# Kernel optimization log

Measured on AMD Instinct MI355X. Metric: run time of the kernel, lower is better.

The kernel has to match this reference:

```python
import jax, jax.numpy as jnp
import numpy as np

B, N_OBJ, N_VAL, E, H, HEADS = 512, 10, 200, 420, 128, 4
NPG = 1 + N_OBJ + N_VAL  # nodes per graph = 211
N = B * NPG
FMIN = float(np.finfo(np.float32).min)


def _gat_conv(x, src, dst, W, att_src, att_dst, bias, concat):
    # PyG GATConv (v1): linear (no bias) -> per-head attention logits ->
    # leaky_relu(a_src[j]+a_dst[i]) -> softmax over edges grouped by dst -> scatter-sum
    heads = att_src.shape[0]
    xs = (x @ W).reshape(N, heads, -1)            # [N, heads, C]
    a_src = (xs * att_src).sum(-1)                # [N, heads]
    a_dst = (xs * att_dst).sum(-1)                # [N, heads]
    alpha = jax.nn.leaky_relu(a_src[src] + a_dst[dst], 0.2)   # [Etot, heads]
    amax = jax.ops.segment_max(alpha, dst, num_segments=N)
    ex = jnp.exp(alpha - amax[dst])
    denom = jax.ops.segment_sum(ex, dst, num_segments=N)
    alpha = ex / (denom[dst] + 1e-16)
    out = jax.ops.segment_sum(xs[src] * alpha[..., None], dst, num_segments=N)  # [N,heads,C]
    out = out.reshape(N, -1) if concat else out.mean(axis=1)
    return out + bias


def setup_inputs() -> dict:
    key = jax.random.key(0)
    ks = jax.random.split(key, 24)
    s = 0.1
    C1 = H // HEADS  # 32
    inp = {
        'head_node': jax.random.normal(ks[0], (B, 2), jnp.float32),
        'objective_nodes': jax.random.normal(ks[1], (B, N_OBJ, 2), jnp.float32),
        'value_nodes': jax.random.normal(ks[2], (B, N_VAL, 5), jnp.float32),
        'edge_indices': jax.random.randint(ks[3], (B, 2, E), 0, NPG, jnp.int64 if jax.config.jax_enable_x64 else jnp.int32),
        'accept_mask': jnp.ones((B, 2), jnp.float32),
        'W_head': jax.random.normal(ks[4], (2, H)) * s, 'b_head': jnp.zeros((H,)),
        'W_obj': jax.random.normal(ks[5], (2, H)) * s, 'b_obj': jnp.zeros((H,)),
        'W_val': jax.random.normal(ks[6], (5, H)) * s, 'b_val': jnp.zeros((H,)),
        'W1': jax.random.normal(ks[7], (H, HEADS * C1)) * s,
        'att_src1': jax.random.normal(ks[8], (HEADS, C1)) * s,
        'att_dst1': jax.random.normal(ks[9], (HEADS, C1)) * s,
        'b1': jnp.zeros((HEADS * C1,)),
        'W2': jax.random.normal(ks[10], (H, HEADS * H)) * s,
        'att_src2': jax.random.normal(ks[11], (HEADS, H)) * s,
        'att_dst2': jax.random.normal(ks[12], (HEADS, H)) * s,
        'b2': jnp.zeros((H,)),
        'W_acc': jax.random.normal(ks[13], (H, 2)) * 0.01, 'b_acc': jnp.zeros((2,)),
        'W_off': jax.random.normal(ks[14], (H, 1)) * 0.01, 'b_off': jnp.zeros((1,)),
        'W_vf': jax.random.normal(ks[15], (H, 1)) * s, 'b_vf': jnp.zeros((1,)),
    }
    return inp


def reference(head_node, objective_nodes, value_nodes, edge_indices, accept_mask,
              W_head, b_head, W_obj, b_obj, W_val, b_val,
              W1, att_src1, att_dst1, b1, W2, att_src2, att_dst2, b2,
              W_acc, b_acc, W_off, b_off, W_vf, b_vf):
    # node encoders + ReLU
    h_head = jax.nn.relu(head_node @ W_head + b_head)                  # [B,H]
    h_obj = jax.nn.relu(objective_nodes @ W_obj + b_obj)               # [B,N_OBJ,H]
    h_val = jax.nn.relu(value_nodes @ W_val + b_val)                   # [B,N_VAL,H]
    h_nodes = jnp.concatenate([h_head[:, None], h_obj, h_val], axis=1)  # [B,NPG,H]
    x = h_nodes.reshape(N, H)
    # batch graphs: offset per-graph edge indices, add self loops
    offs = (jnp.arange(B, dtype=edge_indices.dtype) * NPG)[:, None, None]
    ei = (edge_indices + offs).transpose(1, 0, 2).reshape(2, -1)       # [2, B*E]
    loops = jnp.arange(N, dtype=edge_indices.dtype)
    src = jnp.concatenate([ei[0], loops])
    dst = jnp.concatenate([ei[1], loops])
    # GAT: layer1 concat heads, ReLU (BasicGNN inter-layer act), layer2 mean heads
    x1 = jax.nn.relu(_gat_conv(x, src, dst, W1, att_src1, att_dst1, b1, True))
    x2 = _gat_conv(x1, src, dst, W2, att_src2, att_dst2, b2, False)
    h_out = jax.nn.relu(x2).reshape(B, NPG, H)
    h_head_out = h_out[:, 0]                                           # [B,H]
    h_val_out = h_out[:, -N_VAL:]                                      # [B,N_VAL,H]
    offer_logits = (h_val_out @ W_off + b_off).squeeze(-1)             # [B,N_VAL]
    accept_inf_mask = jnp.maximum(jnp.log(accept_mask), FMIN)
    accept_logits = h_head_out @ W_acc + b_acc + accept_inf_mask       # [B,2]
    vf = h_head_out @ W_vf + b_vf                                      # [B,1]
    return jnp.concatenate([accept_logits, offer_logits, vf], axis=-1)  # [B, 2+N_VAL+1]
```

## Files before the change

kernel.cpp:

```cpp
#include <hip/hip_runtime.h>

typedef unsigned short u16;
typedef unsigned int u32;
typedef short short8 __attribute__((ext_vector_type(8)));
typedef float f32x4 __attribute__((ext_vector_type(4)));

#define NB   512
#define NPG  211
#define NOBJ 10
#define NVAL 200
#define NE   420
#define NN   (NB * NPG)

__device__ __forceinline__ float bf2f(u16 u){
  union { unsigned i; float f; } v; v.i = ((unsigned)u) << 16; return v.f;
}
__device__ __forceinline__ u16 f2bf(float f){
  union { float f; unsigned i; } v; v.f = f;
  return (u16)((v.i + 0x7FFFu + ((v.i >> 16) & 1u)) >> 16);
}
__device__ __forceinline__ float lo_bf(u32 u){ union{u32 i;float f;}v; v.i=u<<16; return v.f; }
__device__ __forceinline__ float hi_bf(u32 u){ union{u32 i;float f;}v; v.i=u&0xffff0000u; return v.f; }
__device__ __forceinline__ u32 pack_bf(float a, float b){ return (u32)f2bf(a) | ((u32)f2bf(b)<<16); }
__device__ __forceinline__ float lrelu(float s){ return s > 0.f ? s : 0.2f * s; }
__device__ __forceinline__ short8 pack8(ushort4 a, ushort4 b){
  short8 v;
  v[0]=(short)a.x; v[1]=(short)a.y; v[2]=(short)a.z; v[3]=(short)a.w;
  v[4]=(short)b.x; v[5]=(short)b.y; v[6]=(short)b.z; v[7]=(short)b.w;
  return v;
}
__device__ __forceinline__ int swz(int r, int c){
  return (r << 7) + (((c & ~3) ^ ((r & 15) << 2)) | (c & 3));
}

__global__ __launch_bounds__(256) void k_prept(const float* __restrict__ W1, const float* __restrict__ W2,
                                               u16* __restrict__ W1t, u16* __restrict__ W2t){
  int gid = blockIdx.x * 256 + threadIdx.x;
  if (gid < 16384){
    int k = gid >> 7, n = gid & 127;
    W1t[n * 128 + k] = f2bf(W1[k * 128 + n]);
  } else {
    int t = gid - 16384;
    int n = t >> 9, kk = t & 511;
    int h = kk >> 7, c = kk & 127;
    W2t[n * 512 + kk] = f2bf(W2[c * 512 + h * 128 + n]);
  }
}

__global__ __launch_bounds__(256) void k_prepwm(const float* __restrict__ W2, const float* __restrict__ as2,
                                                const float* __restrict__ ad2,
                                                float* __restrict__ wms, float* __restrict__ wmd){
  int gid = blockIdx.x * 256 + threadIdx.x;
  int which = gid >> 9, hk = gid & 511;
  int h = hk >> 7, k = hk & 127;
  const float* av = which ? ad2 : as2;
  float s = 0.f;
  for (int j = 0; j < 128; ++j)
    s += W2[k * 512 + h * 128 + j] * av[h * 128 + j];
  (which ? wmd : wms)[hk] = s;
}

__global__ __launch_bounds__(1024, 1) void k_graph(
    const float* __restrict__ head, const float* __restrict__ obj, const float* __restrict__ val,
    const int* __restrict__ eidx, const float* __restrict__ amask,
    const float* __restrict__ Wh, const float* __restrict__ bh,
    const float* __restrict__ Wo, const float* __restrict__ bo,
    const float* __restrict__ Wv, const float* __restrict__ bv,
    const u16* __restrict__ W1t, const float* __restrict__ as1, const float* __restrict__ ad1,
    const float* __restrict__ b1,
    const u16* __restrict__ W2t, const float* __restrict__ wms, const float* __restrict__ wmd,
    const float* __restrict__ b2,
    const float* __restrict__ Wacc, const float* __restrict__ bacc,
    const float* __restrict__ Woff, const float* __restrict__ boff,
    const float* __restrict__ Wvf,  const float* __restrict__ bvf,
    float* __restrict__ out)
{
  __shared__ __align__(16) char sm[135008];
  u16*   sX   = (u16*)sm;
  u16*   sY   = (u16*)(sm + 54016);
  float* sLs  = (float*)(sm + 108032);
  float* sLd  = (float*)(sm + 111408);
  float* sW   = (float*)(sm + 114784);
  float* sDen = (float*)(sm + 124896);
  int*   sEs  = (int*)(sm + 128272);
  int*   sEd  = (int*)(sm + 129952);
  int*   sOff = (int*)(sm + 131632);
  int*   sSrc = (int*)(sm + 132480);

  const int b    = blockIdx.x;
  const int tid  = threadIdx.x;
  const int lane = tid & 63;
  const int wv   = tid >> 6;
  const int l15  = lane & 15;
  const int lg   = lane >> 4;
  const int cp   = lane << 1;
  const int cHi  = cp & ~3, cLo = cp & 3;
  const int hh   = lane >> 4;

  int tmi[4], tcb[4]; bool tact[4];
  #pragma unroll
  for (int s = 0; s < 4; ++s){
    int t = wv + (s << 4);
    tact[s] = t < 56; tmi[s] = t >> 2; tcb[s] = (t & 3) << 5;
  }

  const int* eg = eidx + (size_t)b * 2 * NE;
  if (tid < NE){ sEs[tid] = eg[tid]; sEd[tid] = eg[NE + tid]; }
  else if (tid >= 512 && tid < 640)      sDen[tid - 512] = as1[tid - 512];
  else if (tid >= 640 && tid < 768)      sDen[tid - 512] = ad1[tid - 640];

  for (int it = tid; it < NPG * 32; it += 1024){
    int n = it >> 5, cc = (it & 31) << 2;
    float a[4];
    if (n == 0){
      const float* in = head + (size_t)b * 2;
      float i0 = in[0], i1 = in[1];
      #pragma unroll
      for (int t = 0; t < 4; ++t){ int c = cc + t; a[t] = bh[c] + i0 * Wh[c] + i1 * Wh[128 + c]; }
    } else if (n <= NOBJ){
      const float* in = obj + ((size_t)b * NOBJ + (n - 1)) * 2;
      float i0 = in[0], i1 = in[1];
      #pragma unroll
      for (int t = 0; t < 4; ++t){ int c = cc + t; a[t] = bo[c] + i0 * Wo[c] + i1 * Wo[128 + c]; }
    } else {
      const float* in = val + ((size_t)b * NVAL + (n - 11)) * 5;
      float f[5];
      #pragma unroll
      for (int k = 0; k < 5; ++k) f[k] = in[k];
      #pragma unroll
      for (int t = 0; t < 4; ++t){
        int c = cc + t; float s = bv[c];
        #pragma unroll
        for (int k = 0; k < 5; ++k) s += f[k] * Wv[k * 128 + c];
        a[t] = s;
      }
    }
    ushort4 u;
    u.x = f2bf(fmaxf(a[0], 0.f)); u.y = f2bf(fmaxf(a[1], 0.f));
    u.z = f2bf(fmaxf(a[2], 0.f)); u.w = f2bf(fmaxf(a[3], 0.f));
    *(ushort4*)&sX[swz(n, cc)] = u;
  }
  __syncthreads();

  if (tid < NPG){
    int c = 1;
    const int4* p4 = (const int4*)sEd;
    #pragma unroll 4
    for (int i = 0; i < NE / 4; ++i){
      int4 v = p4[i];
      c += (v.x == tid) + (v.y == tid) + (v.z == tid) + (v.w == tid);
    }
    sOff[tid] = c;
  }
  __syncthreads();
  {
    int deg = (tid < NPG) ? sOff[tid] : 0;
    int v = deg;
    #pragma unroll
    for (int st = 1; st < 256; st <<= 1){
      if (tid < 256) sSrc[tid] = v;
      __syncthreads();
      if (tid < 256 && tid >= st) v += sSrc[tid - st];
      __syncthreads();
    }
    if (tid < NPG) sOff[tid] = v - deg;
    if (tid == NPG - 1) sOff[NPG] = v;
  }
  __syncthreads();
  if (tid < NPG){
    int p = sOff[tid];
    sSrc[p++] = tid;
    const int4* pd4 = (const int4*)sEd;
    const int4* ps4 = (const int4*)sEs;
    for (int i = 0; i < NE / 4; ++i){
      int4 d = pd4[i]; int4 s = ps4[i];
      if (d.x == tid) sSrc[p++] = s.x;
      if (d.y == tid) sSrc[p++] = s.y;
      if (d.z == tid) sSrc[p++] = s.z;
      if (d.w == tid) sSrc[p++] = s.w;
    }
  }
  __syncthreads();

  {
    f32x4 acc[4][2];
    #pragma unroll
    for (int s = 0; s < 4; ++s){ acc[s][0] = (f32x4){0,0,0,0}; acc[s][1] = (f32x4){0,0,0,0}; }
    #pragma unroll
    for (int kk = 0; kk < 4; ++kk){
      int k0 = kk * 32 + (lg << 2);
      #pragma unroll
      for (int s = 0; s < 4; ++s) if (tact[s]){
        const u16* B0 = W1t + (size_t)(tcb[s] + l15) * 128 + k0;
        const u16* B1 = W1t + (size_t)(tcb[s] + 16 + l15) * 128 + k0;
        short8 bf0 = pack8(*(const ushort4*)B0, *(const ushort4*)(B0 + 16));
        short8 bf1 = pack8(*(const ushort4*)B1, *(const ushort4*)(B1 + 16));
        int rr = tmi[s] * 16 + l15; rr = rr < NPG ? rr : NPG - 1;
        short8 af = pack8(*(const ushort4*)&sX[swz(rr, k0)],
                          *(const ushort4*)&sX[swz(rr, k0 + 16)]);
        acc[s][0] = __builtin_amdgcn_mfma_f32_16x16x32_bf16(af, bf0, acc[s][0], 0, 0, 0);
        acc[s][1] = __builtin_amdgcn_mfma_f32_16x16x32_bf16(af, bf1, acc[s][1], 0, 0, 0);
      }
    }
    #pragma unroll
    for (int s = 0; s < 4; ++s) if (tact[s]){
      int r0 = tmi[s] * 16 + (lg << 2);
      #pragma unroll
      for (int ct = 0; ct < 2; ++ct){
        int col = tcb[s] + ct * 16 + l15;
        #pragma unroll
        for (int r = 0; r < 4; ++r){
          int row = r0 + r;
          if (row < NPG) sY[swz(row, col)] = f2bf(acc[s][ct][r]);
        }
      }
    }
  }
  __syncthreads();

  if (tid < NPG * 4){
    int n = tid >> 2, h = tid & 3;
    float s = 0.f, d = 0.f;
    #pragma unroll
    for (int j = 0; j < 8; ++j){
      int c = h * 32 + j * 4;
      ushort4 xv = *(const ushort4*)&sY[swz(n, c)];
      #pragma unroll
      for (int t = 0; t < 4; ++t){
        float xf = bf2f(((const u16*)&xv)[t]);
        s += xf * sDen[c + t];
        d += xf * sDen[128 + c + t];
      }
    }
    sLs[tid] = s; sLd[tid] = d;
  }
  __syncthreads();

  if (tid < NPG * 4){
    int dst = tid >> 2, h = tid & 3;
    int o0 = sOff[dst], o1 = sOff[dst + 1];
    float ad = sLd[tid];
    float m = -3e38f;
    int e = o0;
    for (; e + 4 <= o1; e += 4){
      int s0 = sSrc[e], s1 = sSrc[e+1], s2 = sSrc[e+2], s3 = sSrc[e+3];
      float l0 = sLs[s0*4+h], l1 = sLs[s1*4+h], l2 = sLs[s2*4+h], l3 = sLs[s3*4+h];
      m = fmaxf(m, fmaxf(fmaxf(lrelu(l0+ad), lrelu(l1+ad)), fmaxf(lrelu(l2+ad), lrelu(l3+ad))));
    }
    for (; e < o1; ++e) m = fmaxf(m, lrelu(sLs[sSrc[e]*4+h] + ad));
    float dn = 0.f;
    e = o0;
    for (; e + 4 <= o1; e += 4){
      int s0 = sSrc[e], s1 = sSrc[e+1], s2 = sSrc[e+2], s3 = sSrc[e+3];
      float e0 = __expf(lrelu(sLs[s0*4+h]+ad) - m);
      float e1 = __expf(lrelu(sLs[s1*4+h]+ad) - m);
      float e2 = __expf(lrelu(sLs[s2*4+h]+ad) - m);
      float e3 = __expf(lrelu(sLs[s3*4+h]+ad) - m);
      sW[h*632+e] = e0; sW[h*632+e+1] = e1; sW[h*632+e+2] = e2; sW[h*632+e+3] = e3;
      dn += (e0 + e1) + (e2 + e3);
    }
    for (; e < o1; ++e){
      float ee = __expf(lrelu(sLs[sSrc[e]*4+h]+ad) - m);
      sW[h*632+e] = ee; dn += ee;
    }
    sDen[h * 211 + dst] = 1.0f / (dn + 1e-16f);
  }
  __syncthreads();

  {
    const float b1v0 = b1[cp], b1v1 = b1[cp + 1];
    const float* wp  = sW + hh * 632;
    const float* dnp = sDen + hh * 211;
    for (int dst = wv; dst < NPG; dst += 16){
      int o0 = sOff[dst], o1 = sOff[dst + 1];
      float a0 = 0.f, a1 = 0.f;
      int e = o0;
      for (; e + 4 <= o1; e += 4){
        int s0 = sSrc[e], s1 = sSrc[e+1], s2 = sSrc[e+2], s3 = sSrc[e+3];
        u32 f0 = *(const u32*)&sY[(s0<<7) + (cHi ^ ((s0&15)<<2)) + cLo];
        u32 f1 = *(const u32*)&sY[(s1<<7) + (cHi ^ ((s1&15)<<2)) + cLo];
        u32 f2 = *(const u32*)&sY[(s2<<7) + (cHi ^ ((s2&15)<<2)) + cLo];
        u32 f3 = *(const u32*)&sY[(s3<<7) + (cHi ^ ((s3&15)<<2)) + cLo];
        float w0 = wp[e], w1 = wp[e+1], w2 = wp[e+2], w3 = wp[e+3];
        a0 += w0*lo_bf(f0) + w1*lo_bf(f1) + w2*lo_bf(f2) + w3*lo_bf(f3);
        a1 += w0*hi_bf(f0) + w1*hi_bf(f1) + w2*hi_bf(f2) + w3*hi_bf(f3);
      }
      for (; e < o1; ++e){
        int sn = sSrc[e];
        u32 f = *(const u32*)&sY[(sn<<7) + (cHi ^ ((sn&15)<<2)) + cLo];
        float w = wp[e];
        a0 += w * lo_bf(f); a1 += w * hi_bf(f);
      }
      float r = dnp[dst];
      *(u32*)&sX[(dst<<7) + (cHi ^ ((dst&15)<<2)) + cLo] =
        pack_bf(fmaxf(a0 * r + b1v0, 0.f), fmaxf(a1 * r + b1v1, 0.f));
    }
  }
  __syncthreads();

  sW[tid] = (tid < 512) ? wms[tid] : wmd[tid - 512];
  __syncthreads();

  if (tid < NPG * 4){
    int n = tid >> 2, h = tid & 3;
    const float* wsp = sW + h * 128;
    const float* wdp = sW + 512 + h * 128;
    float s = 0.f, d = 0.f;
    #pragma unroll
    for (int j = 0; j < 32; ++j){
      ushort4 xv = *(const ushort4*)&sX[swz(n, j * 4)];
      #pragma unroll
      for (int t = 0; t < 4; ++t){
        float xf = bf2f(((const u16*)&xv)[t]);
        s += xf * wsp[j * 4 + t];
        d += xf * wdp[j * 4 + t];
      }
    }
    sLs[tid] = s; sLd[tid] = d;
  }
  __syncthreads();

  if (tid < NPG * 4){
    int dst = tid >> 2, h = tid & 3;
    int o0 = sOff[dst], o1 = sOff[dst + 1];
    float ad = sLd[tid];
    float m = -3e38f;
    int e = o0;
    for (; e + 4 <= o1; e += 4){
      int s0 = sSrc[e], s1 = sSrc[e+1], s2 = sSrc[e+2], s3 = sSrc[e+3];
      float l0 = sLs[s0*4+h], l1 = sLs[s1*4+h], l2 = sLs[s2*4+h], l3 = sLs[s3*4+h];
      m = fmaxf(m, fmaxf(fmaxf(lrelu(l0+ad), lrelu(l1+ad)), fmaxf(lrelu(l2+ad), lrelu(l3+ad))));
    }
    for (; e < o1; ++e) m = fmaxf(m, lrelu(sLs[sSrc[e]*4+h] + ad));
    float dn = 0.f;
    e = o0;
    for (; e + 4 <= o1; e += 4){
      int s0 = sSrc[e], s1 = sSrc[e+1], s2 = sSrc[e+2], s3 = sSrc[e+3];
      float e0 = __expf(lrelu(sLs[s0*4+h]+ad) - m);
      float e1 = __expf(lrelu(sLs[s1*4+h]+ad) - m);
      float e2 = __expf(lrelu(sLs[s2*4+h]+ad) - m);
      float e3 = __expf(lrelu(sLs[s3*4+h]+ad) - m);
      sW[h*632+e] = e0; sW[h*632+e+1] = e1; sW[h*632+e+2] = e2; sW[h*632+e+3] = e3;
      dn += (e0 + e1) + (e2 + e3);
    }
    for (; e < o1; ++e){
      float ee = __expf(lrelu(sLs[sSrc[e]*4+h]+ad) - m);
      sW[h*632+e] = ee; dn += ee;
    }
    sDen[h * 211 + dst] = 1.0f / (dn + 1e-16f);
  }
  __syncthreads();

  f32x4 accO[4][2];
  #pragma unroll
  for (int s = 0; s < 4; ++s){ accO[s][0] = (f32x4){0,0,0,0}; accO[s][1] = (f32x4){0,0,0,0}; }
  #pragma unroll 1
  for (int h = 0; h < 4; ++h){
    const float* wp = sW + h * 632;
    for (int dst = wv; dst < NPG; dst += 16){
      int o0 = sOff[dst], o1 = sOff[dst + 1];
      float a0 = 0.f, a1 = 0.f;
      int e = o0;
      for (; e + 4 <= o1; e += 4){
        int s0 = sSrc[e], s1 = sSrc[e+1], s2 = sSrc[e+2], s3 = sSrc[e+3];
        u32 f0 = *(const u32*)&sX[(s0<<7) + (cHi ^ ((s0&15)<<2)) + cLo];
        u32 f1 = *(const u32*)&sX[(s1<<7) + (cHi ^ ((s1&15)<<2)) + cLo];
        u32 f2 = *(const u32*)&sX[(s2<<7) + (cHi ^ ((s2&15)<<2)) + cLo];
        u32 f3 = *(const u32*)&sX[(s3<<7) + (cHi ^ ((s3&15)<<2)) + cLo];
        float w0 = wp[e], w1 = wp[e+1], w2 = wp[e+2], w3 = wp[e+3];
        a0 += w0*lo_bf(f0) + w1*lo_bf(f1) + w2*lo_bf(f2) + w3*lo_bf(f3);
        a1 += w0*hi_bf(f0) + w1*hi_bf(f1) + w2*hi_bf(f2) + w3*hi_bf(f3);
      }
      for (; e < o1; ++e){
        int sn = sSrc[e];
        u32 f = *(const u32*)&sX[(sn<<7) + (cHi ^ ((sn&15)<<2)) + cLo];
        float w = wp[e];
        a0 += w * lo_bf(f); a1 += w * hi_bf(f);
      }
      float sc = 0.25f * sDen[h * 211 + dst];
      *(u32*)&sY[(dst<<7) + (cHi ^ ((dst&15)<<2)) + cLo] = pack_bf(a0 * sc, a1 * sc);
    }
    __syncthreads();
    #pragma unroll
    for (int kk = 0; kk < 4; ++kk){
      int k0 = kk * 32 + (lg << 2);
      #pragma unroll
      for (int s = 0; s < 4; ++s) if (tact[s]){
        const u16* B0 = W2t + (size_t)(tcb[s] + l15) * 512 + h * 128 + k0;
        const u16* B1 = W2t + (size_t)(tcb[s] + 16 + l15) * 512 + h * 128 + k0;
        short8 bf0 = pack8(*(const ushort4*)B0, *(const ushort4*)(B0 + 16));
        short8 bf1 = pack8(*(const ushort4*)B1, *(const ushort4*)(B1 + 16));
        int rr = tmi[s] * 16 + l15; rr = rr < NPG ? rr : NPG - 1;
        short8 af = pack8(*(const ushort4*)&sY[swz(rr, k0)],
                          *(const ushort4*)&sY[swz(rr, k0 + 16)]);
        accO[s][0] = __builtin_amdgcn_mfma_f32_16x16x32_bf16(af, bf0, accO[s][0], 0, 0, 0);
        accO[s][1] = __builtin_amdgcn_mfma_f32_16x16x32_bf16(af, bf1, accO[s][1], 0, 0, 0);
      }
    }
    __syncthreads();
  }

  #pragma unroll
  for (int s = 0; s < 4; ++s) if (tact[s]){
    int r0 = tmi[s] * 16 + (lg << 2);
    #pragma unroll
    for (int ct = 0; ct < 2; ++ct){
      int col = tcb[s] + ct * 16 + l15;
      float bv = b2[col];
      #pragma unroll
      for (int r = 0; r < 4; ++r){
        int row = r0 + r;
        if (row < NPG) sX[swz(row, col)] = f2bf(fmaxf(accO[s][ct][r] + bv, 0.f));
      }
    }
  }
  __syncthreads();

  if (tid < 812){
    int o = tid >> 2, q = tid & 3;
    float s = 0.f;
    if (o < 200){
      int row = 11 + o;
      #pragma unroll
      for (int j = 0; j < 8; ++j){
        int c = q * 32 + j * 4;
        ushort4 xv = *(const ushort4*)&sX[swz(row, c)];
        s += bf2f(xv.x)*Woff[c] + bf2f(xv.y)*Woff[c+1] + bf2f(xv.z)*Woff[c+2] + bf2f(xv.w)*Woff[c+3];
      }
    } else if (o < 202){
      int j2 = o - 200;
      #pragma unroll
      for (int j = 0; j < 8; ++j){
        int c = q * 32 + j * 4;
        ushort4 xv = *(const ushort4*)&sX[swz(0, c)];
        s += bf2f(xv.x)*Wacc[c*2+j2] + bf2f(xv.y)*Wacc[(c+1)*2+j2]
           + bf2f(xv.z)*Wacc[(c+2)*2+j2] + bf2f(xv.w)*Wacc[(c+3)*2+j2];
      }
    } else {
      #pragma unroll
      for (int j = 0; j < 8; ++j){
        int c = q * 32 + j * 4;
        ushort4 xv = *(const ushort4*)&sX[swz(0, c)];
        s += bf2f(xv.x)*Wvf[c] + bf2f(xv.y)*Wvf[c+1] + bf2f(xv.z)*Wvf[c+2] + bf2f(xv.w)*Wvf[c+3];
      }
    }
    s += __shfl_xor(s, 1);
    s += __shfl_xor(s, 2);
    if (q == 0){
      if (o < 200){
        out[(size_t)b * 203 + 2 + o] = s + boff[0];
      } else if (o < 202){
        int j2 = o - 200;
        float lm = logf(amask[b * 2 + j2]);
        out[(size_t)b * 203 + j2] = s + bacc[j2] + fmaxf(lm, -3.402823466e38f);
      } else {
        out[(size_t)b * 203 + 202] = s + bvf[0];
      }
    }
  }
}

extern "C" void kernel_launch(void* const* d_in, const int* in_sizes, int n_in,
                              void* d_out, int out_size, void* d_ws, size_t ws_size,
                              hipStream_t stream){
  (void)in_sizes; (void)n_in; (void)out_size; (void)ws_size;
  const float* head = (const float*)d_in[0];
  const float* obj  = (const float*)d_in[1];
  const float* val  = (const float*)d_in[2];
  const int*   eidx = (const int*)d_in[3];
  const float* amask= (const float*)d_in[4];
  const float* Wh   = (const float*)d_in[5];
  const float* bh   = (const float*)d_in[6];
  const float* Wo   = (const float*)d_in[7];
  const float* bo   = (const float*)d_in[8];
  const float* Wv   = (const float*)d_in[9];
  const float* bv   = (const float*)d_in[10];
  const float* W1   = (const float*)d_in[11];
  const float* as1  = (const float*)d_in[12];
  const float* ad1  = (const float*)d_in[13];
  const float* b1   = (const float*)d_in[14];
  const float* W2   = (const float*)d_in[15];
  const float* as2  = (const float*)d_in[16];
  const float* ad2  = (const float*)d_in[17];
  const float* b2   = (const float*)d_in[18];
  const float* Wacc = (const float*)d_in[19];
  const float* bacc = (const float*)d_in[20];
  const float* Woff = (const float*)d_in[21];
  const float* boff = (const float*)d_in[22];
  const float* Wvf  = (const float*)d_in[23];
  const float* bvf  = (const float*)d_in[24];
  float* out = (float*)d_out;

  char* ws = (char*)d_ws;
  u16*   W1t = (u16*)ws;
  u16*   W2t = (u16*)(ws + 32768);
  float* wms = (float*)(ws + 163840);
  float* wmd = (float*)(ws + 165888);

  k_prept<<<320, 256, 0, stream>>>(W1, W2, W1t, W2t);
  k_prepwm<<<4, 256, 0, stream>>>(W2, as2, ad2, wms, wmd);
  k_graph<<<NB, 1024, 0, stream>>>(head, obj, val, eidx, amask,
                                   Wh, bh, Wo, bo, Wv, bv,
                                   W1t, as1, ad1, b1,
                                   W2t, wms, wmd, b2,
                                   Wacc, bacc, Woff, boff, Wvf, bvf, out);
}
```

Before: 243.7 us.

## Split fused per-graph kernel into multi-kernel global-memory pipeline when workspace allows

Adds a new path that, when the workspace is large enough, replaces the single per-graph kernel (one 1024-thread block per graph with 135KB of LDS) with a chain of smaller kernels: embedding, CSR build, an MFMA GEMM for layer 1, attention logits, softmax, aggregation for both GAT layers, a second GEMM for the W2 projection, and a final head kernel. Intermediates go through global memory in bf16. The aim is to escape the occupancy limit of one huge block per CU and get more parallelism. In exchange it adds many launches and global-memory round trips, about 178MB of workspace. It also removes the 4-way manual unrolling of the edge loops in the fallback kernel.

```diff
diff --git a/kernel.cpp b/kernel.cpp
--- a/kernel.cpp
+++ b/kernel.cpp
@@ -58,6 +58,337 @@
   for (int j = 0; j < 128; ++j)
     s += W2[k * 512 + h * 128 + j] * av[h * 128 + j];
   (which ? wmd : wms)[hk] = s;
+}
+
+
+__global__ __launch_bounds__(256) void k_embed2(
+    const float* __restrict__ head, const float* __restrict__ obj, const float* __restrict__ val,
+    const float* __restrict__ Wh, const float* __restrict__ bh,
+    const float* __restrict__ Wo, const float* __restrict__ bo,
+    const float* __restrict__ Wv, const float* __restrict__ bv,
+    u16* __restrict__ x){
+  int gid = blockIdx.x * 256 + threadIdx.x;
+  int n = gid >> 5, cc = (gid & 31) << 2;
+  int g = n / NPG, loc = n - g * NPG;
+  float a[4];
+  if (loc == 0){
+    const float* in = head + (size_t)g * 2;
+    float i0 = in[0], i1 = in[1];
+    #pragma unroll
+    for (int t = 0; t < 4; ++t){ int c = cc + t; a[t] = bh[c] + i0 * Wh[c] + i1 * Wh[128 + c]; }
+  } else if (loc <= NOBJ){
+    const float* in = obj + ((size_t)g * NOBJ + (loc - 1)) * 2;
+    float i0 = in[0], i1 = in[1];
+    #pragma unroll
+    for (int t = 0; t < 4; ++t){ int c = cc + t; a[t] = bo[c] + i0 * Wo[c] + i1 * Wo[128 + c]; }
+  } else {
+    const float* in = val + ((size_t)g * NVAL + (loc - 11)) * 5;
+    float f[5];
+    #pragma unroll
+    for (int k = 0; k < 5; ++k) f[k] = in[k];
+    #pragma unroll
+    for (int t = 0; t < 4; ++t){
+      int c = cc + t; float s = bv[c];
+      #pragma unroll
+      for (int k = 0; k < 5; ++k) s += f[k] * Wv[k * 128 + c];
+      a[t] = s;
+    }
+  }
+  ushort4 u;
+  u.x = f2bf(fmaxf(a[0], 0.f)); u.y = f2bf(fmaxf(a[1], 0.f));
+  u.z = f2bf(fmaxf(a[2], 0.f)); u.w = f2bf(fmaxf(a[3], 0.f));
+  *(ushort4*)&x[(size_t)n * 128 + cc] = u;
+}
+
+__global__ __launch_bounds__(256) void k_csr2(const int* __restrict__ eidx,
+                                              int* __restrict__ coff, int* __restrict__ csrc){
+  __shared__ int sEs[420], sEd[420], sTmp[256], sOff[212], sSrc[632];
+  int g = blockIdx.x, tid = threadIdx.x;
+  const int4* e4 = (const int4*)(eidx + (size_t)g * 840);
+  for (int i = tid; i < 105; i += 256){ ((int4*)sEs)[i] = e4[i]; ((int4*)sEd)[i] = e4[105 + i]; }
+  __syncthreads();
+  int deg = 0;
+  if (tid < NPG){
+    deg = 1;
+    const int4* p4 = (const int4*)sEd;
+    #pragma unroll 4
+    for (int i = 0; i < 105; ++i){
+      int4 v = p4[i];
+      deg += (v.x == tid) + (v.y == tid) + (v.z == tid) + (v.w == tid);
+    }
+  }
+  int v = deg;
+  #pragma unroll
+  for (int st = 1; st < 256; st <<= 1){
+    sTmp[tid] = v;
+    __syncthreads();
+    if (tid >= st) v += sTmp[tid - st];
+    __syncthreads();
+  }
+  if (tid < NPG) sOff[tid] = v - deg;
+  if (tid == NPG - 1) sOff[NPG] = v;
+  __syncthreads();
+  if (tid < NPG){
+    int p = sOff[tid];
+    sSrc[p++] = tid;
+    const int4* pd4 = (const int4*)sEd;
+    const int4* ps4 = (const int4*)sEs;
+    for (int i = 0; i < 105; ++i){
+      int4 d = pd4[i]; int4 s = ps4[i];
+      if (d.x == tid) sSrc[p++] = s.x;
+      if (d.y == tid) sSrc[p++] = s.y;
+      if (d.z == tid) sSrc[p++] = s.z;
+      if (d.w == tid) sSrc[p++] = s.w;
+    }
+  }
+  __syncthreads();
+  if (tid < 212) coff[(size_t)g * 212 + tid] = sOff[tid];
+  for (int i = tid; i < 631; i += 256) csrc[(size_t)g * 632 + i] = sSrc[i];
+}
+
+template<int KCH, bool RELU>
+__global__ __launch_bounds__(256) void k_mm(const u16* __restrict__ A, size_t chunkStride,
+                                            const u16* __restrict__ Bt, int bstride,
+                                            const float* __restrict__ bias, u16* __restrict__ C){
+  __shared__ u16 sA[128 * 128];
+  const int tid = threadIdx.x, lane = tid & 63, w = tid >> 6;
+  const int l15 = lane & 15, lg = lane >> 4;
+  const int row0 = blockIdx.x * 128;
+  f32x4 acc[2][8];
+  #pragma unroll
+  for (int mi = 0; mi < 2; ++mi)
+    #pragma unroll
+    for (int ni = 0; ni < 8; ++ni) acc[mi][ni] = (f32x4){0,0,0,0};
+
+  #pragma unroll 1
+  for (int ch = 0; ch < KCH; ++ch){
+    const u16* Ab = A + (size_t)ch * chunkStride + (size_t)row0 * 128;
+    #pragma unroll
+    for (int q0 = 0; q0 < 2048; q0 += 256){
+      int q = q0 + tid;
+      int r = q >> 4, c8 = (q & 15) << 3;
+      ushort4 v0 = *(const ushort4*)(Ab + r * 128 + c8);
+      ushort4 v1 = *(const ushort4*)(Ab + r * 128 + c8 + 4);
+      *(ushort4*)&sA[swz(r, c8)]     = v0;
+      *(ushort4*)&sA[swz(r, c8 + 4)] = v1;
+    }
+    __syncthreads();
+    #pragma unroll
+    for (int kk = 0; kk < 4; ++kk){
+      int k0 = kk * 32 + (lg << 2);
+      short8 af[2];
+      #pragma unroll
+      for (int mi = 0; mi < 2; ++mi){
+        int rr = (w * 2 + mi) * 16 + l15;
+        af[mi] = pack8(*(const ushort4*)&sA[swz(rr, k0)],
+                       *(const ushort4*)&sA[swz(rr, k0 + 16)]);
+      }
+      #pragma unroll
+      for (int ni = 0; ni < 8; ++ni){
+        const u16* Bp = Bt + (size_t)(ni * 16 + l15) * bstride + ch * 128 + k0;
+        short8 bf = pack8(*(const ushort4*)Bp, *(const ushort4*)(Bp + 16));
+        acc[0][ni] = __builtin_amdgcn_mfma_f32_16x16x32_bf16(af[0], bf, acc[0][ni], 0, 0, 0);
+        acc[1][ni] = __builtin_amdgcn_mfma_f32_16x16x32_bf16(af[1], bf, acc[1][ni], 0, 0, 0);
+      }
+    }
+    __syncthreads();
+  }
+  #pragma unroll
+  for (int mi = 0; mi < 2; ++mi){
+    int r0 = row0 + (w * 2 + mi) * 16 + (lg << 2);
+    #pragma unroll
+    for (int ni = 0; ni < 8; ++ni){
+      int col = ni * 16 + l15;
+      float bv = RELU ? bias[col] : 0.f;
+      #pragma unroll
+      for (int r = 0; r < 4; ++r){
+        float v = acc[mi][ni][r];
+        if (RELU) v = fmaxf(v + bv, 0.f);
+        C[(size_t)(r0 + r) * 128 + col] = f2bf(v);
+      }
+    }
+  }
+}
+
+__global__ __launch_bounds__(256) void k_att1k(const u16* __restrict__ xs1,
+                                               const float* __restrict__ as1, const float* __restrict__ ad1,
+                                               float* __restrict__ Ls, float* __restrict__ Ld){
+  int t = blockIdx.x * 256 + threadIdx.x;
+  int n = t >> 2, h = t & 3;
+  const u16* xr = xs1 + (size_t)n * 128 + h * 32;
+  float s = 0.f, d = 0.f;
+  #pragma unroll
+  for (int j = 0; j < 8; ++j){
+    ushort4 xv = *(const ushort4*)(xr + j * 4);
+    #pragma unroll
+    for (int q = 0; q < 4; ++q){
+      float xf = bf2f(((const u16*)&xv)[q]);
+      int c = h * 32 + j * 4 + q;
+      s += xf * as1[c];
+      d += xf * ad1[c];
+    }
+  }
+  Ls[t] = s; Ld[t] = d;
+}
+
+__global__ __launch_bounds__(256) void k_att2k(const u16* __restrict__ x1,
+                                               const float* __restrict__ wms, const float* __restrict__ wmd,
+                                               float* __restrict__ Ls, float* __restrict__ Ld){
+  __shared__ float sw[1024];
+  int tid = threadIdx.x;
+  for (int i = tid; i < 512; i += 256) sw[i] = wms[i];
+  for (int i = tid; i < 512; i += 256) sw[512 + i] = wmd[i];
+  __syncthreads();
+  int t = blockIdx.x * 256 + tid;
+  int n = t >> 2, h = t & 3;
+  const u16* xr = x1 + (size_t)n * 128;
+  const float* wsp = sw + h * 128;
+  const float* wdp = sw + 512 + h * 128;
+  float s = 0.f, d = 0.f;
+  #pragma unroll
+  for (int j = 0; j < 32; ++j){
+    ushort4 xv = *(const ushort4*)(xr + j * 4);
+    #pragma unroll
+    for (int q = 0; q < 4; ++q){
+      float xf = bf2f(((const u16*)&xv)[q]);
+      s += xf * wsp[j * 4 + q];
+      d += xf * wdp[j * 4 + q];
+    }
+  }
+  Ls[t] = s; Ld[t] = d;
+}
+
+__global__ __launch_bounds__(256) void k_smk(const float* __restrict__ Ls, const float* __restrict__ Ld,
+                                             const int* __restrict__ coff, const int* __restrict__ csrc,
+                                             float* __restrict__ wn, float* __restrict__ rden, float fold){
+  int g = blockIdx.x >> 2;
+  int t = ((blockIdx.x & 3) << 8) + threadIdx.x;
+  if (t >= NPG * 4) return;
+  int dst = t >> 2, h = t & 3;
+  int gb = g * NPG;
+  int o0 = coff[(size_t)g * 212 + dst], o1 = coff[(size_t)g * 212 + dst + 1];
+  const int* sp = csrc + (size_t)g * 632;
+  float ad = Ld[(size_t)(gb + dst) * 4 + h];
+  float m = -3e38f;
+  for (int e = o0; e < o1; ++e) m = fmaxf(m, lrelu(Ls[(size_t)(gb + sp[e]) * 4 + h] + ad));
+  float dn = 0.f;
+  float* wp = wn + (size_t)g * 2528 + h * 632;
+  for (int e = o0; e < o1; ++e){
+    float ee = __expf(lrelu(Ls[(size_t)(gb + sp[e]) * 4 + h] + ad) - m);
+    wp[e] = ee; dn += ee;
+  }
+  rden[(size_t)(gb + dst) * 4 + h] = fold / (dn + 1e-16f);
+}
+
+__global__ __launch_bounds__(256) void k_gat1k(const u16* __restrict__ xs1,
+                                               const float* __restrict__ wn, const float* __restrict__ rden,
+                                               const int* __restrict__ coff, const int* __restrict__ csrc,
+                                               const float* __restrict__ b1, u16* __restrict__ x1){
+  int bid = blockIdx.x;
+  int g = bid / 53, ch = bid - g * 53;
+  int dst = ch * 4 + (threadIdx.x >> 6);
+  if (dst >= NPG) return;
+  int lane = threadIdx.x & 63;
+  int cp = lane << 1, hh = lane >> 4;
+  int gb = g * NPG;
+  int o0 = coff[(size_t)g * 212 + dst], o1 = coff[(size_t)g * 212 + dst + 1];
+  const int* sp = csrc + (size_t)g * 632;
+  const float* wp = wn + (size_t)g * 2528 + hh * 632;
+  float a0 = 0.f, a1 = 0.f;
+  for (int e = o0; e < o1; ++e){
+    int src = sp[e];
+    u32 f = *(const u32*)&xs1[(size_t)(gb + src) * 128 + cp];
+    float w = wp[e];
+    a0 += w * lo_bf(f); a1 += w * hi_bf(f);
+  }
+  float rv = rden[(size_t)(gb + dst) * 4 + hh];
+  *(u32*)&x1[(size_t)(gb + dst) * 128 + cp] =
+    pack_bf(fmaxf(a0 * rv + b1[cp], 0.f), fmaxf(a1 * rv + b1[cp + 1], 0.f));
+}
+
+__global__ __launch_bounds__(256) void k_gat2k(const u16* __restrict__ x1,
+                                               const float* __restrict__ wn, const float* __restrict__ rden,
+                                               const int* __restrict__ coff, const int* __restrict__ csrc,
+                                               u16* __restrict__ y){
+  int bid = blockIdx.x;
+  int g = bid / 53, ch = bid - g * 53;
+  int dst = ch * 4 + (threadIdx.x >> 6);
+  if (dst >= NPG) return;
+  int lane = threadIdx.x & 63;
+  int cp = lane << 1;
+  int gb = g * NPG;
+  int o0 = coff[(size_t)g * 212 + dst], o1 = coff[(size_t)g * 212 + dst + 1];
+  const int* sp = csrc + (size_t)g * 632;
+  const float* wb = wn + (size_t)g * 2528;
+  float a0[4] = {0,0,0,0}, a1[4] = {0,0,0,0};
+  for (int e = o0; e < o1; ++e){
+    int src = sp[e];
+    u32 f = *(const u32*)&x1[(size_t)(gb + src) * 128 + cp];
+    float xl = lo_bf(f), xh = hi_bf(f);
+    #pragma unroll
+    for (int h = 0; h < 4; ++h){
+      float w = wb[h * 632 + e];
+      a0[h] += w * xl; a1[h] += w * xh;
+    }
+  }
+  #pragma unroll
+  for (int h = 0; h < 4; ++h){
+    float rv = rden[(size_t)(gb + dst) * 4 + h];
+    *(u32*)&y[(size_t)h * NN * 128 + (size_t)(gb + dst) * 128 + cp] =
+      pack_bf(a0[h] * rv, a1[h] * rv);
+  }
+}
+
+__global__ __launch_bounds__(256) void k_final2(const u16* __restrict__ out2, const float* __restrict__ amask,
+                                                const float* __restrict__ Wacc, const float* __restrict__ bacc,
+                                                const float* __restrict__ Woff, const float* __restrict__ boff,
+                                                const float* __restrict__ Wvf,  const float* __restrict__ bvf,
+                                                float* __restrict__ out){
+  int g = blockIdx.x >> 2;
+  int t = ((blockIdx.x & 3) << 8) + threadIdx.x;
+  if (t >= 812) return;
+  int o = t >> 2, q = t & 3;
+  float s = 0.f;
+  if (o < 200){
+    const u16* row = out2 + (size_t)(g * NPG + 11 + o) * 128;
+    #pragma unroll
+    for (int j = 0; j < 8; ++j){
+      int c = q * 32 + j * 4;
+      ushort4 xv = *(const ushort4*)(row + c);
+      s += bf2f(xv.x)*Woff[c] + bf2f(xv.y)*Woff[c+1] + bf2f(xv.z)*Woff[c+2] + bf2f(xv.w)*Woff[c+3];
+    }
+  } else if (o < 202){
+    int j2 = o - 200;
+    const u16* row = out2 + (size_t)(g * NPG) * 128;
+    #pragma unroll
+    for (int j = 0; j < 8; ++j){
+      int c = q * 32 + j * 4;
+      ushort4 xv = *(const ushort4*)(row + c);
+      s += bf2f(xv.x)*Wacc[c*2+j2] + bf2f(xv.y)*Wacc[(c+1)*2+j2]
+         + bf2f(xv.z)*Wacc[(c+2)*2+j2] + bf2f(xv.w)*Wacc[(c+3)*2+j2];
+    }
+  } else {
+    const u16* row = out2 + (size_t)(g * NPG) * 128;
+    #pragma unroll
+    for (int j = 0; j < 8; ++j){
+      int c = q * 32 + j * 4;
+      ushort4 xv = *(const ushort4*)(row + c);
+      s += bf2f(xv.x)*Wvf[c] + bf2f(xv.y)*Wvf[c+1] + bf2f(xv.z)*Wvf[c+2] + bf2f(xv.w)*Wvf[c+3];
+    }
+  }
+  s += __shfl_xor(s, 1);
+  s += __shfl_xor(s, 2);
+  if (q == 0){
+    if (o < 200){
+      out[(size_t)g * 203 + 2 + o] = s + boff[0];
+    } else if (o < 202){
+      int j2 = o - 200;
+      float lm = logf(amask[g * 2 + j2]);
+      out[(size_t)g * 203 + j2] = s + bacc[j2] + fmaxf(lm, -3.402823466e38f);
+    } else {
+      out[(size_t)g * 203 + 202] = s + bvf[0];
+    }
+  }
 }
 
 __global__ __launch_bounds__(1024, 1) void k_graph(
@@ -241,27 +572,11 @@
     int o0 = sOff[dst], o1 = sOff[dst + 1];
     float ad = sLd[tid];
     float m = -3e38f;
-    int e = o0;
-    for (; e + 4 <= o1; e += 4){
-      int s0 = sSrc[e], s1 = sSrc[e+1], s2 = sSrc[e+2], s3 = sSrc[e+3];
-      float l0 = sLs[s0*4+h], l1 = sLs[s1*4+h], l2 = sLs[s2*4+h], l3 = sLs[s3*4+h];
-      m = fmaxf(m, fmaxf(fmaxf(lrelu(l0+ad), lrelu(l1+ad)), fmaxf(lrelu(l2+ad), lrelu(l3+ad))));
-    }
-    for (; e < o1; ++e) m = fmaxf(m, lrelu(sLs[sSrc[e]*4+h] + ad));
+    for (int e = o0; e < o1; ++e) m = fmaxf(m, lrelu(sLs[sSrc[e] * 4 + h] + ad));
     float dn = 0.f;
-    e = o0;
-    for (; e + 4 <= o1; e += 4){
-      int s0 = sSrc[e], s1 = sSrc[e+1], s2 = sSrc[e+2], s3 = sSrc[e+3];
-      float e0 = __expf(lrelu(sLs[s0*4+h]+ad) - m);
-      float e1 = __expf(lrelu(sLs[s1*4+h]+ad) - m);
-      float e2 = __expf(lrelu(sLs[s2*4+h]+ad) - m);
-      float e3 = __expf(lrelu(sLs[s3*4+h]+ad) - m);
-      sW[h*632+e] = e0; sW[h*632+e+1] = e1; sW[h*632+e+2] = e2; sW[h*632+e+3] = e3;
-      dn += (e0 + e1) + (e2 + e3);
-    }
-    for (; e < o1; ++e){
-      float ee = __expf(lrelu(sLs[sSrc[e]*4+h]+ad) - m);
-      sW[h*632+e] = ee; dn += ee;
+    for (int e = o0; e < o1; ++e){
+      float ee = __expf(lrelu(sLs[sSrc[e] * 4 + h] + ad) - m);
+      sW[h * 632 + e] = ee; dn += ee;
     }
     sDen[h * 211 + dst] = 1.0f / (dn + 1e-16f);
   }
@@ -274,18 +589,7 @@
     for (int dst = wv; dst < NPG; dst += 16){
       int o0 = sOff[dst], o1 = sOff[dst + 1];
       float a0 = 0.f, a1 = 0.f;
-      int e = o0;
-      for (; e + 4 <= o1; e += 4){
-        int s0 = sSrc[e], s1 = sSrc[e+1], s2 = sSrc[e+2], s3 = sSrc[e+3];
-        u32 f0 = *(const u32*)&sY[(s0<<7) + (cHi ^ ((s0&15)<<2)) + cLo];
-        u32 f1 = *(const u32*)&sY[(s1<<7) + (cHi ^ ((s1&15)<<2)) + cLo];
-        u32 f2 = *(const u32*)&sY[(s2<<7) + (cHi ^ ((s2&15)<<2)) + cLo];
-        u32 f3 = *(const u32*)&sY[(s3<<7) + (cHi ^ ((s3&15)<<2)) + cLo];
-        float w0 = wp[e], w1 = wp[e+1], w2 = wp[e+2], w3 = wp[e+3];
-        a0 += w0*lo_bf(f0) + w1*lo_bf(f1) + w2*lo_bf(f2) + w3*lo_bf(f3);
-        a1 += w0*hi_bf(f0) + w1*hi_bf(f1) + w2*hi_bf(f2) + w3*hi_bf(f3);
-      }
-      for (; e < o1; ++e){
+      for (int e = o0; e < o1; ++e){
         int sn = sSrc[e];
         u32 f = *(const u32*)&sY[(sn<<7) + (cHi ^ ((sn&15)<<2)) + cLo];
         float w = wp[e];
@@ -325,27 +629,11 @@
     int o0 = sOff[dst], o1 = sOff[dst + 1];
     float ad = sLd[tid];
     float m = -3e38f;
-    int e = o0;
-    for (; e + 4 <= o1; e += 4){
-      int s0 = sSrc[e], s1 = sSrc[e+1], s2 = sSrc[e+2], s3 = sSrc[e+3];
-      float l0 = sLs[s0*4+h], l1 = sLs[s1*4+h], l2 = sLs[s2*4+h], l3 = sLs[s3*4+h];
-      m = fmaxf(m, fmaxf(fmaxf(lrelu(l0+ad), lrelu(l1+ad)), fmaxf(lrelu(l2+ad), lrelu(l3+ad))));
-    }
-    for (; e < o1; ++e) m = fmaxf(m, lrelu(sLs[sSrc[e]*4+h] + ad));
+    for (int e = o0; e < o1; ++e) m = fmaxf(m, lrelu(sLs[sSrc[e] * 4 + h] + ad));
     float dn = 0.f;
-    e = o0;
-    for (; e + 4 <= o1; e += 4){
-      int s0 = sSrc[e], s1 = sSrc[e+1], s2 = sSrc[e+2], s3 = sSrc[e+3];
-      float e0 = __expf(lrelu(sLs[s0*4+h]+ad) - m);
-      float e1 = __expf(lrelu(sLs[s1*4+h]+ad) - m);
-      float e2 = __expf(lrelu(sLs[s2*4+h]+ad) - m);
-      float e3 = __expf(lrelu(sLs[s3*4+h]+ad) - m);
-      sW[h*632+e] = e0; sW[h*632+e+1] = e1; sW[h*632+e+2] = e2; sW[h*632+e+3] = e3;
-      dn += (e0 + e1) + (e2 + e3);
-    }
-    for (; e < o1; ++e){
-      float ee = __expf(lrelu(sLs[sSrc[e]*4+h]+ad) - m);
-      sW[h*632+e] = ee; dn += ee;
+    for (int e = o0; e < o1; ++e){
+      float ee = __expf(lrelu(sLs[sSrc[e] * 4 + h] + ad) - m);
+      sW[h * 632 + e] = ee; dn += ee;
     }
     sDen[h * 211 + dst] = 1.0f / (dn + 1e-16f);
   }
@@ -360,18 +648,7 @@
     for (int dst = wv; dst < NPG; dst += 16){
       int o0 = sOff[dst], o1 = sOff[dst + 1];
       float a0 = 0.f, a1 = 0.f;
-      int e = o0;
-      for (; e + 4 <= o1; e += 4){
-        int s0 = sSrc[e], s1 = sSrc[e+1], s2 = sSrc[e+2], s3 = sSrc[e+3];
-        u32 f0 = *(const u32*)&sX[(s0<<7) + (cHi ^ ((s0&15)<<2)) + cLo];
-        u32 f1 = *(const u32*)&sX[(s1<<7) + (cHi ^ ((s1&15)<<2)) + cLo];
-        u32 f2 = *(const u32*)&sX[(s2<<7) + (cHi ^ ((s2&15)<<2)) + cLo];
-        u32 f3 = *(const u32*)&sX[(s3<<7) + (cHi ^ ((s3&15)<<2)) + cLo];
-        float w0 = wp[e], w1 = wp[e+1], w2 = wp[e+2], w3 = wp[e+3];
-        a0 += w0*lo_bf(f0) + w1*lo_bf(f1) + w2*lo_bf(f2) + w3*lo_bf(f3);
-        a1 += w0*hi_bf(f0) + w1*hi_bf(f1) + w2*hi_bf(f2) + w3*hi_bf(f3);
-      }
-      for (; e < o1; ++e){
+      for (int e = o0; e < o1; ++e){
         int sn = sSrc[e];
         u32 f = *(const u32*)&sX[(sn<<7) + (cHi ^ ((sn&15)<<2)) + cLo];
         float w = wp[e];
@@ -463,7 +740,7 @@
 extern "C" void kernel_launch(void* const* d_in, const int* in_sizes, int n_in,
                               void* d_out, int out_size, void* d_ws, size_t ws_size,
                               hipStream_t stream){
-  (void)in_sizes; (void)n_in; (void)out_size; (void)ws_size;
+  (void)in_sizes; (void)n_in; (void)out_size;
   const float* head = (const float*)d_in[0];
   const float* obj  = (const float*)d_in[1];
   const float* val  = (const float*)d_in[2];
@@ -499,9 +776,35 @@
 
   k_prept<<<320, 256, 0, stream>>>(W1, W2, W1t, W2t);
   k_prepwm<<<4, 256, 0, stream>>>(W2, as2, ad2, wms, wmd);
-  k_graph<<<NB, 1024, 0, stream>>>(head, obj, val, eidx, amask,
-                                   Wh, bh, Wo, bo, Wv, bv,
-                                   W1t, as1, ad1, b1,
-                                   W2t, wms, wmd, b2,
-                                   Wacc, bacc, Woff, boff, Wvf, bvf, out);
-}
+
+  const size_t NEED = 178196480;
+  if (ws_size >= NEED){
+    int*   coff = (int*)(ws + 167936);
+    int*   csrc = (int*)(ws + 602112);
+    float* aLs  = (float*)(ws + 1896448);
+    float* aLd  = (float*)(ws + 3624960);
+    float* wn   = (float*)(ws + 5353472);
+    float* rden = (float*)(ws + 10530816);
+    u16*   x    = (u16*)(ws + 12259328);
+    u16*   xs1  = (u16*)(ws + 39915520);
+    u16*   y    = (u16*)(ws + 67571712);
+
+    k_embed2<<<NN * 32 / 256, 256, 0, stream>>>(head, obj, val, Wh, bh, Wo, bo, Wv, bv, x);
+    k_csr2<<<NB, 256, 0, stream>>>(eidx, coff, csrc);
+    k_mm<1, false><<<NN / 128, 256, 0, stream>>>(x, 0, W1t, 128, nullptr, xs1);
+    k_att1k<<<NN * 4 / 256, 256, 0, stream>>>(xs1, as1, ad1, aLs, aLd);
+    k_smk<<<NB * 4, 256, 0, stream>>>(aLs, aLd, coff, csrc, wn, rden, 1.0f);
+    k_gat1k<<<NB * 53, 256, 0, stream>>>(xs1, wn, rden, coff, csrc, b1, x);
+    k_att2k<<<NN * 4 / 256, 256, 0, stream>>>(x, wms, wmd, aLs, aLd);
+    k_smk<<<NB * 4, 256, 0, stream>>>(aLs, aLd, coff, csrc, wn, rden, 0.25f);
+    k_gat2k<<<NB * 53, 256, 0, stream>>>(x, wn, rden, coff, csrc, y);
+    k_mm<4, true><<<NN / 128, 256, 0, stream>>>(y, (size_t)NN * 128, W2t, 512, b2, xs1);
+    k_final2<<<NB * 4, 256, 0, stream>>>(xs1, amask, Wacc, bacc, Woff, boff, Wvf, bvf, out);
+  } else {
+    k_graph<<<NB, 1024, 0, stream>>>(head, obj, val, eidx, amask,
+                                     Wh, bh, Wo, bo, Wv, bv,
+                                     W1t, as1, ad1, b1,
+                                     W2t, wms, wmd, b2,
+                                     Wacc, bacc, Woff, boff, Wvf, bvf, out);
+  }
+}
```

Result: slower. 389.0 us (+59.6%).
